# Optimization experiments

Measured on AMD Instinct MI355X. Metric: run time of the kernel, lower is better.

Reference implementation:

```python
import jax, jax.numpy as jnp
import numpy as np

D, L, C, H, W = 4, 16, 64, 128, 128


def setup_inputs() -> dict:
    key = jax.random.key(0)
    ks = jax.random.split(key, 20)
    rn = lambda k, shape, s=0.02: jax.random.normal(k, shape, dtype=jnp.float32) * s
    return {
        "x": jax.random.normal(ks[0], (L, C, H, W), dtype=jnp.float32),
        "ln1_g": jnp.ones((D, C, H, W), jnp.float32),
        "ln1_b": jnp.zeros((D, C, H, W), jnp.float32),
        "Wq": rn(ks[1], (D, C, C)), "bq": jnp.zeros((D, C), jnp.float32),
        "Wk": rn(ks[2], (D, C, C)), "bk": jnp.zeros((D, C), jnp.float32),
        "Wv": rn(ks[3], (D, C, C)), "bv": jnp.zeros((D, C), jnp.float32),
        "Wa": rn(ks[4], (D, 1, 2 * C, 5, 5)), "ba": jnp.zeros((D, 1), jnp.float32),
        "ln2_g": jnp.ones((D, C, H, W), jnp.float32),
        "ln2_b": jnp.zeros((D, C, H, W), jnp.float32),
        "W1": rn(ks[5], (D, 2 * C, C)), "b1": jnp.zeros((D, 2 * C), jnp.float32),
        "W2": rn(ks[6], (D, C, 2 * C)), "b2": jnp.zeros((D, C), jnp.float32),
    }


def _layernorm(x, g, b):
    # torch nn.LayerNorm([C,H,W]): normalize over last 3 dims per frame, eps=1e-5
    mu = jnp.mean(x, axis=(1, 2, 3), keepdims=True)
    var = jnp.var(x, axis=(1, 2, 3), keepdims=True)
    return (x - mu) * jax.lax.rsqrt(var + 1e-5) * g[None] + b[None]


def _conv5(x, w):
    # x: [L, Cin, H, W], w: [1, Cin, 5, 5] -> [L, 1, H, W], SAME padding (pad=2)
    return jax.lax.conv_general_dilated(
        x, w, window_strides=(1, 1), padding="SAME",
        dimension_numbers=("NCHW", "OIHW", "NCHW"))


def _conv1x1(x, w, b):
    # 1x1 conv == per-pixel linear over channels
    return jnp.einsum("lchw,oc->lohw", x, w) + b[None, :, None, None]


def reference(x, ln1_g, ln1_b, Wq, bq, Wk, bk, Wv, bv, Wa, ba,
              ln2_g, ln2_b, W1, b1, W2, b2):
    depth = ln1_g.shape[0]
    c = Wa.shape[2] // 2
    for d in range(depth):
        # --- pre-norm conv attention (nheads=1) + residual ---
        h = _layernorm(x, ln1_g[d], ln1_b[d])
        Q = _conv1x1(h, Wq[d], bq[d])
        K = _conv1x1(h, Wk[d], bk[d])
        V = _conv1x1(h, Wv[d], bv[d])
        # conv_atten(cat([Q_i, K_j])) is linear in channels: split the 5x5
        # kernel into Q-part and K-part, so H_ij = A_i + B_j + bias.
        A = _conv5(Q, Wa[d, :, :c])[:, 0]   # [L, H, W]
        B = _conv5(K, Wa[d, :, c:])[:, 0]   # [L, H, W]
        S = A[:, None] + B[None, :] + ba[d][0]      # [L, L, H, W]
        P = jax.nn.softmax(S, axis=1)               # softmax over source frames j
        attn = jnp.einsum("ijhw,jchw->ichw", P, V)  # weighted sum of V_j
        x = x + attn
        # --- pre-norm conv FFN + residual ---
        h = _layernorm(x, ln2_g[d], ln2_b[d])
        f = _conv1x1(h, W1[d], b1[d])
        f = jax.nn.leaky_relu(f, 0.01)  # torch LeakyReLU default slope
        f = _conv1x1(f, W2[d], b2[d])
        x = x + f
    return x
```

## Files before the change

### kernel.cpp

```cpp
#include <hip/hip_runtime.h>


#define HW 16384
#define CHW 1048576
#define NB 64

typedef unsigned short u16;
typedef __attribute__((ext_vector_type(8))) short bf16x8;
typedef __attribute__((ext_vector_type(8))) unsigned short u16x8;
typedef __attribute__((ext_vector_type(4))) float f32x4;

static __device__ __forceinline__ u16 f2bf(float f) {
  union { float f; unsigned int u; } v; v.f = f;
  unsigned int r = v.u + 0x7fffu + ((v.u >> 16) & 1u);
  return (u16)(r >> 16);
}
static __device__ __forceinline__ float bf2f(u16 h) {
  union { unsigned int u; float f; } v; v.u = ((unsigned int)h) << 16;
  return v.f;
}
static __device__ __forceinline__ void ln_from_acc_wave(
    const float* acc, int l, int lane, float& mu, float& r) {
  const float invN = 1.f / 1048576.f;
  float2 v = *(const float2*)(acc + lane * 32 + 2 * l);
  float s = v.x, q = v.y;
#pragma unroll
  for (int off = 32; off > 0; off >>= 1) {
    s += __shfl_xor(s, off);
    q += __shfl_xor(q, off);
  }
  mu = s * invN;
  r = rsqrtf(q * invN - mu * mu + 1e-5f);
}

__global__ __launch_bounds__(256) void prep_kernel(
    const float* __restrict__ Wa, const float* __restrict__ Wk,
    const float* __restrict__ Wv, const float* __restrict__ W1,
    const float* __restrict__ W2, u16* __restrict__ w1pk,
    u16* __restrict__ w2pk, u16* __restrict__ wvpk, u16* __restrict__ wepk) {
  int d = blockIdx.x;
  int t = blockIdx.y * 256 + threadIdx.x;
  const int STR = 256 * 16;
  const float* WaK = Wa + ((size_t)d * 128 + 64) * 25;
  const float* Wkd = Wk + d * 4096;
  for (int idx = t; idx < 2048; idx += STR) {
    int frag = idx >> 9, lane = (idx >> 3) & 63, j = idx & 7;
    int mt = frag >> 1, kt = frag & 1;
    int tap = mt * 16 + (lane & 15);
    int ci = kt * 32 + (lane >> 4) * 8 + j;
    float s = 0.f;
    if (tap < 25)
      for (int co = 0; co < 64; ++co)
        s = fmaf(WaK[co * 25 + tap], Wkd[co * 64 + ci], s);
    wepk[d * 2048 + idx] = f2bf(s);
  }
  const float* Wvd = Wv + d * 4096;
  for (int idx = t; idx < 4096; idx += STR) {
    int frag = idx >> 9, lane = (idx >> 3) & 63, j = idx & 7;
    int mt = frag >> 1, kt = frag & 1;
    int co = mt * 16 + (lane & 15);
    int ci = kt * 32 + (lane >> 4) * 8 + j;
    wvpk[d * 4096 + idx] = f2bf(Wvd[co * 64 + ci]);
  }
  const float* W1d = W1 + d * 8192;
  for (int idx = t; idx < 8192; idx += STR) {
    int frag = idx >> 9, lane = (idx >> 3) & 63, j = idx & 7;
    int mt = frag >> 1, kt = frag & 1;
    int o = mt * 16 + (lane & 15);
    int ci = kt * 32 + (lane >> 4) * 8 + j;
    w1pk[d * 8192 + idx] = f2bf(W1d[o * 64 + ci]);
  }
  const float* W2d = W2 + d * 8192;
  for (int idx = t; idx < 8192; idx += STR) {
    int frag = idx >> 9, lane = (idx >> 3) & 63, j = idx & 7;
    int mt2 = frag >> 2, kt2 = frag & 3;
    int c = mt2 * 16 + (lane & 15);
    int o = kt2 * 32 + (lane >> 4) * 8 + j;
    w2pk[d * 8192 + idx] = f2bf(W2d[c * 128 + o]);
  }
}

__global__ __launch_bounds__(256) void lngb_kernel(
    const float* __restrict__ g1, u16* __restrict__ o1) {
  int idx = blockIdx.x * 256 + threadIdx.x;
  float4 v = *(const float4*)(g1 + (size_t)idx * 4);
  ushort4 o;
  o.x = f2bf(v.x); o.y = f2bf(v.y); o.z = f2bf(v.z); o.w = f2bf(v.w);
  *(ushort4*)(o1 + (size_t)idx * 4) = o;
}

__global__ __launch_bounds__(256) void stats_kernel(
    const float* __restrict__ xin, float* __restrict__ acc) {
  int tid = threadIdx.x;
  size_t base = (size_t)blockIdx.x * 4096;
  const float4* in4 = (const float4*)(xin + base);
  float s = 0.f, q = 0.f;
#pragma unroll
  for (int k = 0; k < 4; ++k) {
    float4 v = in4[k * 256 + tid];
    s += v.x + v.y + v.z + v.w;
    q = fmaf(v.x, v.x, q); q = fmaf(v.y, v.y, q);
    q = fmaf(v.z, v.z, q); q = fmaf(v.w, v.w, q);
  }
#pragma unroll
  for (int off = 32; off > 0; off >>= 1) {
    s += __shfl_down(s, off); q += __shfl_down(q, off);
  }
  __shared__ float ls[4], lq[4];
  int wave = tid >> 6;
  if ((tid & 63) == 0) { ls[wave] = s; lq[wave] = q; }
  __syncthreads();
  if (tid == 0) {
    int frame = blockIdx.x >> 8;
    int bkt = blockIdx.x & (NB - 1);
    atomicAdd(&acc[bkt * 32 + frame * 2], ls[0] + ls[1] + ls[2] + ls[3]);
    atomicAdd(&acc[bkt * 32 + frame * 2 + 1], lq[0] + lq[1] + lq[2] + lq[3]);
  }
}

__global__ __launch_bounds__(256) void tb_kernel(
    const float* __restrict__ x, const u16* __restrict__ g,
    const float* __restrict__ bln, const u16* __restrict__ wep_g,
    const float* __restrict__ accA, float* __restrict__ accBz,
    float* __restrict__ mulr, u16* __restrict__ T) {
  __shared__ __align__(16) char lds[18432];
  u16* hb = (u16*)lds;
  int tid = threadIdx.x;
  int l = blockIdx.y;
  int p0 = blockIdx.x << 7;
  if (blockIdx.x == 0 && blockIdx.y == 0)
    for (int i = tid; i < NB * 32; i += 256) accBz[i] = 0.f;
  int lane = tid & 63;
  float mu, r;
  ln_from_acc_wave(accA, l, lane, mu, r);
  if (blockIdx.x == 0 && tid == 0) {
    mulr[2 * l] = mu;
    mulr[2 * l + 1] = r;
  }

  {
    int pq = tid & 15, cg = tid >> 4;
    int px0 = pq * 8, c0 = cg * 4;
    float vv[4][8];
#pragma unroll
    for (int i = 0; i < 4; ++i) {
      int c = c0 + i;
      size_t gi = (((size_t)l * 64 + c) << 14) + p0 + px0;
      int li = (c << 14) + p0 + px0;
      float4 xv0 = *(const float4*)(x + gi);
      float4 xv1 = *(const float4*)(x + gi + 4);
      u16x8 gv = *(const u16x8*)(g + li);
      float4 bb0 = *(const float4*)(bln + li);
      float4 bb1 = *(const float4*)(bln + li + 4);
#pragma unroll
      for (int k = 0; k < 8; ++k) {
        float xk = k < 4 ? ((const float*)&xv0)[k] : ((const float*)&xv1)[k - 4];
        float bbk = k < 4 ? ((const float*)&bb0)[k] : ((const float*)&bb1)[k - 4];
        vv[i][k] = (xk - mu) * r * bf2f(gv[k]) + bbk;
      }
    }
#pragma unroll
    for (int k = 0; k < 8; ++k) {
      int row = px0 + k;
      int col = ((((c0 >> 3) + (row >> 2)) & 7) << 3) | (c0 & 7);
      ushort4 hv;
      hv.x = f2bf(vv[0][k]); hv.y = f2bf(vv[1][k]);
      hv.z = f2bf(vv[2][k]); hv.w = f2bf(vv[3][k]);
      *(ushort4*)(hb + row * 72 + col) = hv;
    }
  }
  __syncthreads();

  int wv = tid >> 6;
  int ln15 = lane & 15, quad = lane >> 4;

  bf16x8 ah[2][2];
#pragma unroll
  for (int mt = 0; mt < 2; ++mt) {
    int px = (wv * 2 + mt) * 16 + ln15;
#pragma unroll
    for (int kt = 0; kt < 2; ++kt) {
      int slot = ((kt * 4 + quad) + (px >> 2)) & 7;
      ah[mt][kt] = *(const bf16x8*)(hb + px * 72 + (slot << 3));
    }
  }
  const bf16x8* weg = (const bf16x8*)wep_g;

  f32x4 accT[2][2];
#pragma unroll
  for (int mt = 0; mt < 2; ++mt)
#pragma unroll
    for (int nt = 0; nt < 2; ++nt) accT[mt][nt] = (f32x4){0.f, 0.f, 0.f, 0.f};
#pragma unroll
  for (int nt = 0; nt < 2; ++nt) {
    bf16x8 b0 = weg[(nt * 2 + 0) * 64 + lane];
    bf16x8 b1w = weg[(nt * 2 + 1) * 64 + lane];
#pragma unroll
    for (int mt = 0; mt < 2; ++mt) {
      accT[mt][nt] = __builtin_amdgcn_mfma_f32_16x16x32_bf16(
          ah[mt][0], b0, accT[mt][nt], 0, 0, 0);
      accT[mt][nt] = __builtin_amdgcn_mfma_f32_16x16x32_bf16(
          ah[mt][1], b1w, accT[mt][nt], 0, 0, 0);
    }
  }

#pragma unroll
  for (int mt = 0; mt < 2; ++mt) {
    int pxb = p0 + (wv * 2 + mt) * 16 + quad * 4;
#pragma unroll
    for (int nt = 0; nt < 2; ++nt) {
      int tap = nt * 16 + ln15;
      if (tap < 25) {
        ushort4 o;
        o.x = f2bf(accT[mt][nt][0]); o.y = f2bf(accT[mt][nt][1]);
        o.z = f2bf(accT[mt][nt][2]); o.w = f2bf(accT[mt][nt][3]);
        *(ushort4*)(T + (((size_t)l * 25 + tap) << 14) + pxb) = o;
      }
    }
  }
}

__global__ __launch_bounds__(256) void attnc_kernel(
    const float* __restrict__ x, const u16* __restrict__ T,
    const u16* __restrict__ g1, const float* __restrict__ b1g,
    const u16* __restrict__ wvp_g, const float* __restrict__ bv,
    const float* __restrict__ mulr, u16* __restrict__ abf) {
  __shared__ float Bsm[16][68];
  __shared__ float Prl[16][64];
  __shared__ float scal[64];
  __shared__ __align__(16) u16 hb[64 * 72];
  int tid = threadIdx.x;
  int p0 = blockIdx.x << 6;

  {
    int j = tid >> 4, xg = tid & 15;
    int y0 = p0 >> 7, x0 = p0 & 127;
    float acc4[4] = {0.f, 0.f, 0.f, 0.f};
    const u16* Tj = T + (((size_t)j * 25) << 14);
#pragma unroll
    for (int dy = 0; dy < 5; ++dy) {
      int yy = y0 + dy - 2;
      if (yy < 0 || yy > 127) continue;
#pragma unroll
      for (int dx = 0; dx < 5; ++dx) {
        const u16* Tt = Tj + ((dy * 5 + dx) << 14) + (yy << 7);
#pragma unroll
        for (int k = 0; k < 4; ++k) {
          int xc = x0 + xg * 4 + k + dx - 2;
          if (xc >= 0 && xc < 128) acc4[k] += bf2f(Tt[xc]);
        }
      }
    }
#pragma unroll
    for (int k = 0; k < 4; ++k) Bsm[j][xg * 4 + k] = acc4[k];
  }
  __syncthreads();

  if (tid < 64) {
    float bj[16], m = -1e30f;
#pragma unroll
    for (int j = 0; j < 16; ++j) {
      bj[j] = Bsm[j][tid];
      m = fmaxf(m, bj[j]);
    }
    float sum = 0.f;
#pragma unroll
    for (int j = 0; j < 16; ++j) {
      bj[j] = __expf(bj[j] - m);
      sum += bj[j];
    }
    float inv = 1.f / sum;
    float sc = 0.f;
#pragma unroll
    for (int j = 0; j < 16; ++j) {
      float mu_j = mulr[2 * j], r_j = mulr[2 * j + 1];
      float prl = bj[j] * inv * r_j;
      Prl[j][tid] = prl;
      sc = fmaf(prl, mu_j, sc);
    }
    scal[tid] = sc;
  }
  __syncthreads();

  {
    int c2 = tid >> 3, pxg = tid & 7;
    int px0 = pxg * 8;
    float xbar[2][8];
#pragma unroll
    for (int cc = 0; cc < 2; ++cc)
#pragma unroll
      for (int k = 0; k < 8; ++k) xbar[cc][k] = 0.f;
#pragma unroll
    for (int j = 0; j < 16; ++j) {
      float p8[8];
#pragma unroll
      for (int k = 0; k < 8; ++k) p8[k] = Prl[j][px0 + k];
#pragma unroll
      for (int cc = 0; cc < 2; ++cc) {
        int c = cc * 32 + c2;
        const float* xp = x + (((size_t)j * 64 + c) << 14) + p0 + px0;
        float4 xv0 = *(const float4*)xp;
        float4 xv1 = *(const float4*)(xp + 4);
#pragma unroll
        for (int k = 0; k < 8; ++k) {
          float xk =
              k < 4 ? ((const float*)&xv0)[k] : ((const float*)&xv1)[k - 4];
          xbar[cc][k] = fmaf(p8[k], xk, xbar[cc][k]);
        }
      }
    }
    float sc8[8];
#pragma unroll
    for (int k = 0; k < 8; ++k) sc8[k] = scal[px0 + k];
#pragma unroll
    for (int cc = 0; cc < 2; ++cc) {
      int c = cc * 32 + c2;
      int li = (c << 14) + p0 + px0;
      u16x8 g8 = *(const u16x8*)(g1 + li);
      float4 b0 = *(const float4*)(b1g + li);
      float4 b1v = *(const float4*)(b1g + li + 4);
#pragma unroll
      for (int k = 0; k < 8; ++k) {
        float bbk = k < 4 ? ((const float*)&b0)[k] : ((const float*)&b1v)[k - 4];
        float hv = bf2f(g8[k]) * (xbar[cc][k] - sc8[k]) + bbk;
        int row = px0 + k;
        int col = ((((c >> 3) + (row >> 2)) & 7) << 3) | (c & 7);
        hb[row * 72 + col] = f2bf(hv);
      }
    }
  }
  __syncthreads();

  int wv = tid >> 6, lane = tid & 63;
  int ln15 = lane & 15, quad = lane >> 4;
  int px = wv * 16 + ln15;
  bf16x8 ah[2];
#pragma unroll
  for (int kt = 0; kt < 2; ++kt) {
    int slot = ((kt * 4 + quad) + (px >> 2)) & 7;
    ah[kt] = *(const bf16x8*)(hb + px * 72 + (slot << 3));
  }
  const bf16x8* wvg = (const bf16x8*)wvp_g;
  f32x4 accV[4];
#pragma unroll
  for (int nt = 0; nt < 4; ++nt) accV[nt] = (f32x4){0.f, 0.f, 0.f, 0.f};
#pragma unroll
  for (int nt = 0; nt < 4; ++nt) {
    bf16x8 b0 = wvg[(nt * 2 + 0) * 64 + lane];
    bf16x8 b1w = wvg[(nt * 2 + 1) * 64 + lane];
    accV[nt] = __builtin_amdgcn_mfma_f32_16x16x32_bf16(ah[0], b0, accV[nt],
                                                       0, 0, 0);
    accV[nt] = __builtin_amdgcn_mfma_f32_16x16x32_bf16(ah[1], b1w, accV[nt],
                                                       0, 0, 0);
  }
  int pxb = p0 + wv * 16 + quad * 4;
#pragma unroll
  for (int nt = 0; nt < 4; ++nt) {
    int c = nt * 16 + ln15;
    float bvc = bv[c];
    ushort4 o;
    o.x = f2bf(accV[nt][0] + bvc);
    o.y = f2bf(accV[nt][1] + bvc);
    o.z = f2bf(accV[nt][2] + bvc);
    o.w = f2bf(accV[nt][3] + bvc);
    *(ushort4*)(abf + ((size_t)c << 14) + pxb) = o;
  }
}

__global__ __launch_bounds__(256) void stats2_kernel(
    const float* __restrict__ x, const u16* __restrict__ abf,
    float* __restrict__ accB, float* __restrict__ accAz) {
  int tid = threadIdx.x;
  if (blockIdx.x == 0)
    for (int i = tid; i < NB * 32; i += 256) accAz[i] = 0.f;
  size_t base = (size_t)blockIdx.x * 4096;
  int intra = (blockIdx.x & 255) * 4096;
  float s = 0.f, q = 0.f;
#pragma unroll
  for (int k = 0; k < 4; ++k) {
    int off = (k * 256 + tid) * 4;
    float4 v = *(const float4*)(x + base + off);
    ushort4 a4 = *(const ushort4*)(abf + intra + off);
    float v0 = v.x + bf2f(a4.x), v1 = v.y + bf2f(a4.y);
    float v2 = v.z + bf2f(a4.z), v3 = v.w + bf2f(a4.w);
    s += v0 + v1 + v2 + v3;
    q = fmaf(v0, v0, q); q = fmaf(v1, v1, q);
    q = fmaf(v2, v2, q); q = fmaf(v3, v3, q);
  }
#pragma unroll
  for (int off = 32; off > 0; off >>= 1) {
    s += __shfl_down(s, off); q += __shfl_down(q, off);
  }
  __shared__ float ls[4], lq[4];
  int wave = tid >> 6;
  if ((tid & 63) == 0) { ls[wave] = s; lq[wave] = q; }
  __syncthreads();
  if (tid == 0) {
    int frame = blockIdx.x >> 8;
    int bkt = blockIdx.x & (NB - 1);
    atomicAdd(&accB[bkt * 32 + frame * 2], ls[0] + ls[1] + ls[2] + ls[3]);
    atomicAdd(&accB[bkt * 32 + frame * 2 + 1], lq[0] + lq[1] + lq[2] + lq[3]);
  }
}

__global__ __launch_bounds__(256) void ffn_kernel(
    const float* __restrict__ xr, float* __restrict__ xw,
    const u16* __restrict__ ap, const float* __restrict__ g,
    const float* __restrict__ bln, const u16* __restrict__ w1p_g,
    const float* __restrict__ b1, const u16* __restrict__ w2p_g,
    const float* __restrict__ b2, const float* __restrict__ accB,
    float* __restrict__ accA) {
  __shared__ __align__(16) char lds[66560];
  float* xaf = (float*)lds;
  u16* hb = (u16*)(lds + 33792);
  u16* f1 = (u16*)(lds + 33792);

  int tid = threadIdx.x;
  int P0 = blockIdx.x << 7;
  int l = P0 >> 14;
  int p0 = P0 & 16383;
  int lane = tid & 63;
  float mu, r;
  ln_from_acc_wave(accB, l, lane, mu, r);

#pragma unroll
  for (int it = 0; it < 2; ++it) {
    int pq = tid & 31, cg = (tid >> 5) + it * 8;
    int px = pq * 4, c0 = cg * 4;
    float vv[4][4];
#pragma unroll
    for (int i = 0; i < 4; ++i) {
      int c = c0 + i;
      size_t gi = (((size_t)l * 64 + c) << 14) + p0 + px;
      int li = (c << 14) + p0 + px;
      float4 xv = *(const float4*)(xr + gi);
      ushort4 av4 = *(const ushort4*)(ap + li);
      float4 gv = *(const float4*)(g + li);
      float4 bb = *(const float4*)(bln + li);
      float4 s4;
      s4.x = xv.x + bf2f(av4.x); s4.y = xv.y + bf2f(av4.y);
      s4.z = xv.z + bf2f(av4.z); s4.w = xv.w + bf2f(av4.w);
      *(float4*)(xaf + c * 132 + px) = s4;
      vv[i][0] = (s4.x - mu) * r * gv.x + bb.x;
      vv[i][1] = (s4.y - mu) * r * gv.y + bb.y;
      vv[i][2] = (s4.z - mu) * r * gv.z + bb.z;
      vv[i][3] = (s4.w - mu) * r * gv.w + bb.w;
    }
#pragma unroll
    for (int k = 0; k < 4; ++k) {
      int row = px + k;
      int col = ((((c0 >> 3) + (row >> 2)) & 7) << 3) | (c0 & 7);
      ushort4 hv;
      hv.x = f2bf(vv[0][k]); hv.y = f2bf(vv[1][k]);
      hv.z = f2bf(vv[2][k]); hv.w = f2bf(vv[3][k]);
      *(ushort4*)(hb + row * 72 + col) = hv;
    }
  }
  __syncthreads();

  int wv = tid >> 6;
  int ln15 = lane & 15, quad = lane >> 4;

  bf16x8 bh[2][2];
#pragma unroll
  for (int nt = 0; nt < 2; ++nt) {
    int px = (wv * 2 + nt) * 16 + ln15;
#pragma unroll
    for (int kt = 0; kt < 2; ++kt) {
      int slot = ((kt * 4 + quad) + (px >> 2)) & 7;
      bh[nt][kt] = *(const bf16x8*)(hb + px * 72 + (slot << 3));
    }
  }
  __syncthreads();

  const bf16x8* w1g = (const bf16x8*)w1p_g;
  const bf16x8* w2g = (const bf16x8*)w2p_g;

#pragma unroll
  for (int mt = 0; mt < 8; ++mt) {
    bf16x8 a1a = w1g[(mt * 2 + 0) * 64 + lane];
    bf16x8 a1b = w1g[(mt * 2 + 1) * 64 + lane];
    f32x4 acc[2];
    acc[0] = (f32x4){0.f, 0.f, 0.f, 0.f};
    acc[1] = (f32x4){0.f, 0.f, 0.f, 0.f};
#pragma unroll
    for (int nt = 0; nt < 2; ++nt) {
      acc[nt] = __builtin_amdgcn_mfma_f32_16x16x32_bf16(a1a, bh[nt][0],
                                                        acc[nt], 0, 0, 0);
      acc[nt] = __builtin_amdgcn_mfma_f32_16x16x32_bf16(a1b, bh[nt][1],
                                                        acc[nt], 0, 0, 0);
    }
    int o0 = mt * 16 + quad * 4;
    float4 b1v = *(const float4*)(b1 + o0);
#pragma unroll
    for (int nt = 0; nt < 2; ++nt) {
      int px = (wv * 2 + nt) * 16 + ln15;
      int swz = (px & 7) * 8;
      float fv[4];
#pragma unroll
      for (int rj = 0; rj < 4; ++rj) {
        float f = acc[nt][rj] + ((const float*)&b1v)[rj];
        fv[rj] = fmaxf(f, 0.01f * f);
      }
      int col = ((o0 & ~7) ^ swz) + (o0 & 7);
      ushort4 ov;
      ov.x = f2bf(fv[0]); ov.y = f2bf(fv[1]);
      ov.z = f2bf(fv[2]); ov.w = f2bf(fv[3]);
      *(ushort4*)(f1 + px * 128 + col) = ov;
    }
  }
  __syncthreads();

  bf16x8 a2[2][4];
#pragma unroll
  for (int mt = 0; mt < 2; ++mt) {
    int px = (wv * 2 + mt) * 16 + ln15;
    int swz = (px & 7) * 8;
#pragma unroll
    for (int kt = 0; kt < 4; ++kt)
      a2[mt][kt] =
          *(const bf16x8*)(f1 + px * 128 + ((kt * 32 + quad * 8) ^ swz));
  }
  f32x4 acc2[2][4];
#pragma unroll
  for (int mt = 0; mt < 2; ++mt)
#pragma unroll
    for (int nt = 0; nt < 4; ++nt) acc2[mt][nt] = (f32x4){0.f, 0.f, 0.f, 0.f};
#pragma unroll
  for (int nt = 0; nt < 4; ++nt) {
    bf16x8 bw[4];
#pragma unroll
    for (int kt = 0; kt < 4; ++kt) bw[kt] = w2g[(nt * 4 + kt) * 64 + lane];
#pragma unroll
    for (int mt = 0; mt < 2; ++mt)
#pragma unroll
      for (int kt = 0; kt < 4; ++kt)
        acc2[mt][nt] = __builtin_amdgcn_mfma_f32_16x16x32_bf16(
            a2[mt][kt], bw[kt], acc2[mt][nt], 0, 0, 0);
  }

  float s = 0.f, q = 0.f;
#pragma unroll
  for (int mt = 0; mt < 2; ++mt) {
    int pxl = (wv * 2 + mt) * 16 + quad * 4;
#pragma unroll
    for (int nt = 0; nt < 4; ++nt) {
      int c = nt * 16 + ln15;
      float b2c = b2[c];
      const float* xac = xaf + c * 132 + pxl;
      float4 v;
      v.x = xac[0] + acc2[mt][nt][0] + b2c;
      v.y = xac[1] + acc2[mt][nt][1] + b2c;
      v.z = xac[2] + acc2[mt][nt][2] + b2c;
      v.w = xac[3] + acc2[mt][nt][3] + b2c;
      *(float4*)(xw + (((size_t)l * 64 + c) << 14) + p0 + pxl) = v;
      s += v.x + v.y + v.z + v.w;
      q = fmaf(v.x, v.x, q); q = fmaf(v.y, v.y, q);
      q = fmaf(v.z, v.z, q); q = fmaf(v.w, v.w, q);
    }
  }
#pragma unroll
  for (int off = 32; off > 0; off >>= 1) {
    s += __shfl_down(s, off); q += __shfl_down(q, off);
  }
  if (lane == 0) {
    int bkt = blockIdx.x & (NB - 1);
    atomicAdd(&accA[bkt * 32 + l * 2], s);
    atomicAdd(&accA[bkt * 32 + l * 2 + 1], q);
  }
}

extern "C" void kernel_launch(void* const* d_in, const int* in_sizes, int n_in,
                              void* d_out, int out_size, void* d_ws,
                              size_t ws_size, hipStream_t stream) {
  const float* x_in = (const float*)d_in[0];
  const float* ln1_g = (const float*)d_in[1];
  const float* ln1_b = (const float*)d_in[2];
  const float* Wk = (const float*)d_in[5];
  const float* Wv = (const float*)d_in[7];
  const float* bv = (const float*)d_in[8];
  const float* Wa = (const float*)d_in[9];
  const float* ln2_g = (const float*)d_in[11];
  const float* ln2_b = (const float*)d_in[12];
  const float* W1 = (const float*)d_in[13];
  const float* b1 = (const float*)d_in[14];
  const float* W2 = (const float*)d_in[15];
  const float* b2 = (const float*)d_in[16];

  float* xbuf = (float*)d_out;
  char* wsb = (char*)d_ws;
  u16* T = (u16*)wsb;
  u16* abf = (u16*)(wsb + 13107200);
  u16* g1b = (u16*)(wsb + 15204352);
  u16* w1pk = (u16*)(wsb + 23592960);
  u16* w2pk = (u16*)(wsb + 23658496);
  u16* wvpk = (u16*)(wsb + 23724032);
  u16* wepk = (u16*)(wsb + 23756800);
  float* mulr = (float*)(wsb + 23773184);
  float* accA = (float*)(wsb + 23773312);
  float* accB = (float*)(wsb + 23781504);

  hipMemsetAsync(accA, 0, 16384, stream);
  prep_kernel<<<dim3(4, 16), 256, 0, stream>>>(Wa, Wk, Wv, W1, W2, w1pk, w2pk,
                                               wvpk, wepk);
  lngb_kernel<<<4096, 256, 0, stream>>>(ln1_g, g1b);
  stats_kernel<<<4096, 256, 0, stream>>>(x_in, accA);

  const float* xr = x_in;
  for (int d = 0; d < 4; ++d) {
    tb_kernel<<<dim3(128, 16), 256, 0, stream>>>(
        xr, g1b + (size_t)d * CHW, ln1_b + (size_t)d * CHW, wepk + d * 2048,
        accA, accB, mulr, T);
    attnc_kernel<<<256, 256, 0, stream>>>(
        xr, T, g1b + (size_t)d * CHW, ln1_b + (size_t)d * CHW,
        wvpk + d * 4096, bv + d * 64, mulr, abf);
    stats2_kernel<<<4096, 256, 0, stream>>>(xr, abf, accB, accA);
    ffn_kernel<<<2048, 256, 0, stream>>>(
        xr, xbuf, abf, ln2_g + (size_t)d * CHW, ln2_b + (size_t)d * CHW,
        w1pk + d * 8192, b1 + d * 128, w2pk + d * 8192, b2 + d * 64, accB,
        accA);
    xr = xbuf;
  }
}
```

Before: 569.7 us.

## Switch activations and LN params to channels-last layout across all kernels

Transposes x once into a channels-last (pixel-major, channel-contiguous) workspace buffer and converts all four LayerNorm gamma/beta tensors to channels-last bf16 up front. Each per-layer kernel (tb, attnc, stats2, ffn) now reads and writes contiguous channel vectors per pixel, and the MFMA operands are swapped so outputs land channel-contiguous. The aim is vectorized coalesced loads and simpler LDS staging without per-element transposes, and bf16 beta halves its traffic. The cost is an extra transpose kernel, a larger workspace, a strided channel-major write in the last FFN, and bf16 rounding of the LN biases.

```diff
diff --git a/kernel.cpp b/kernel.cpp
--- a/kernel.cpp
+++ b/kernel.cpp
@@ -4,6 +4,8 @@
 #define HW 16384
 #define CHW 1048576
 #define NB 64
+
+#define XI(l, p, c) ((((size_t)(l)) << 20) + (size_t)(p)*64 + (c))
 
 typedef unsigned short u16;
 typedef __attribute__((ext_vector_type(8))) short bf16x8;
@@ -80,47 +82,100 @@
   }
 }
 
-__global__ __launch_bounds__(256) void lngb_kernel(
-    const float* __restrict__ g1, u16* __restrict__ o1) {
-  int idx = blockIdx.x * 256 + threadIdx.x;
-  float4 v = *(const float4*)(g1 + (size_t)idx * 4);
-  ushort4 o;
-  o.x = f2bf(v.x); o.y = f2bf(v.y); o.z = f2bf(v.z); o.w = f2bf(v.w);
-  *(ushort4*)(o1 + (size_t)idx * 4) = o;
-}
-
-__global__ __launch_bounds__(256) void stats_kernel(
-    const float* __restrict__ xin, float* __restrict__ acc) {
+__global__ __launch_bounds__(256) void pcl_kernel(
+    const float* __restrict__ g1, const float* __restrict__ b1,
+    const float* __restrict__ g2, const float* __restrict__ b2,
+    u16* __restrict__ g1cl, u16* __restrict__ b1cl, u16* __restrict__ g2cl,
+    u16* __restrict__ b2cl) {
+  __shared__ float tl[128][65];
   int tid = threadIdx.x;
-  size_t base = (size_t)blockIdx.x * 4096;
-  const float4* in4 = (const float4*)(xin + base);
+  int y = blockIdx.x;
+  int tsel = blockIdx.y >> 2, d = blockIdx.y & 3;
+  const float* src;
+  u16* dst;
+  switch (tsel) {
+    case 0: src = g1; dst = g1cl; break;
+    case 1: src = b1; dst = b1cl; break;
+    case 2: src = g2; dst = g2cl; break;
+    default: src = b2; dst = b2cl; break;
+  }
+  src += (size_t)d * CHW;
+  dst += (size_t)d * CHW;
+  {
+    int c = tid >> 2, xg = tid & 3;
+    const float* sp = src + (size_t)c * HW + y * 128 + xg * 32;
+#pragma unroll
+    for (int k = 0; k < 8; ++k) {
+      float4 v = *(const float4*)(sp + k * 4);
+      int xx = xg * 32 + k * 4;
+      tl[xx + 0][c] = v.x; tl[xx + 1][c] = v.y;
+      tl[xx + 2][c] = v.z; tl[xx + 3][c] = v.w;
+    }
+  }
+  __syncthreads();
+  {
+    int px = tid >> 1, c0 = (tid & 1) << 5;
+    u16* dp = dst + (size_t)(y * 128 + px) * 64 + c0;
+#pragma unroll
+    for (int k = 0; k < 4; ++k) {
+      u16x8 o;
+#pragma unroll
+      for (int e = 0; e < 8; ++e) o[e] = f2bf(tl[px][c0 + k * 8 + e]);
+      *(u16x8*)(dp + k * 8) = o;
+    }
+  }
+}
+
+__global__ __launch_bounds__(256) void xpose_kernel(
+    const float* __restrict__ xin, float* __restrict__ xcl,
+    float* __restrict__ acc) {
+  __shared__ float tl[128][65];
+  __shared__ float ls[4], lq[4];
+  int tid = threadIdx.x;
+  int l = blockIdx.x >> 7, y = blockIdx.x & 127;
   float s = 0.f, q = 0.f;
-#pragma unroll
-  for (int k = 0; k < 4; ++k) {
-    float4 v = in4[k * 256 + tid];
-    s += v.x + v.y + v.z + v.w;
-    q = fmaf(v.x, v.x, q); q = fmaf(v.y, v.y, q);
-    q = fmaf(v.z, v.z, q); q = fmaf(v.w, v.w, q);
+  {
+    int c = tid >> 2, xg = tid & 3;
+    const float* sp = xin + (size_t)l * CHW + (size_t)c * HW + y * 128 + xg * 32;
+#pragma unroll
+    for (int k = 0; k < 8; ++k) {
+      float4 v = *(const float4*)(sp + k * 4);
+      int xx = xg * 32 + k * 4;
+      tl[xx + 0][c] = v.x; tl[xx + 1][c] = v.y;
+      tl[xx + 2][c] = v.z; tl[xx + 3][c] = v.w;
+      s += v.x + v.y + v.z + v.w;
+      q = fmaf(v.x, v.x, q); q = fmaf(v.y, v.y, q);
+      q = fmaf(v.z, v.z, q); q = fmaf(v.w, v.w, q);
+    }
+  }
+  __syncthreads();
+  {
+    int px = tid >> 1, c0 = (tid & 1) << 5;
+    float* dp = xcl + XI(l, y * 128 + px, c0);
+#pragma unroll
+    for (int k = 0; k < 8; ++k) {
+      float4 w = {tl[px][c0 + k * 4 + 0], tl[px][c0 + k * 4 + 1],
+                  tl[px][c0 + k * 4 + 2], tl[px][c0 + k * 4 + 3]};
+      *(float4*)(dp + k * 4) = w;
+    }
   }
 #pragma unroll
   for (int off = 32; off > 0; off >>= 1) {
     s += __shfl_down(s, off); q += __shfl_down(q, off);
   }
-  __shared__ float ls[4], lq[4];
   int wave = tid >> 6;
   if ((tid & 63) == 0) { ls[wave] = s; lq[wave] = q; }
   __syncthreads();
   if (tid == 0) {
-    int frame = blockIdx.x >> 8;
     int bkt = blockIdx.x & (NB - 1);
-    atomicAdd(&acc[bkt * 32 + frame * 2], ls[0] + ls[1] + ls[2] + ls[3]);
-    atomicAdd(&acc[bkt * 32 + frame * 2 + 1], lq[0] + lq[1] + lq[2] + lq[3]);
+    atomicAdd(&acc[bkt * 32 + l * 2], ls[0] + ls[1] + ls[2] + ls[3]);
+    atomicAdd(&acc[bkt * 32 + l * 2 + 1], lq[0] + lq[1] + lq[2] + lq[3]);
   }
 }
 
 __global__ __launch_bounds__(256) void tb_kernel(
-    const float* __restrict__ x, const u16* __restrict__ g,
-    const float* __restrict__ bln, const u16* __restrict__ wep_g,
+    const float* __restrict__ xcl, const u16* __restrict__ g,
+    const u16* __restrict__ bln, const u16* __restrict__ wep_g,
     const float* __restrict__ accA, float* __restrict__ accBz,
     float* __restrict__ mulr, u16* __restrict__ T) {
   __shared__ __align__(16) char lds[18432];
@@ -139,34 +194,24 @@
   }
 
   {
-    int pq = tid & 15, cg = tid >> 4;
-    int px0 = pq * 8, c0 = cg * 4;
-    float vv[4][8];
-#pragma unroll
-    for (int i = 0; i < 4; ++i) {
-      int c = c0 + i;
-      size_t gi = (((size_t)l * 64 + c) << 14) + p0 + px0;
-      int li = (c << 14) + p0 + px0;
-      float4 xv0 = *(const float4*)(x + gi);
-      float4 xv1 = *(const float4*)(x + gi + 4);
-      u16x8 gv = *(const u16x8*)(g + li);
-      float4 bb0 = *(const float4*)(bln + li);
-      float4 bb1 = *(const float4*)(bln + li + 4);
-#pragma unroll
-      for (int k = 0; k < 8; ++k) {
-        float xk = k < 4 ? ((const float*)&xv0)[k] : ((const float*)&xv1)[k - 4];
-        float bbk = k < 4 ? ((const float*)&bb0)[k] : ((const float*)&bb1)[k - 4];
-        vv[i][k] = (xk - mu) * r * bf2f(gv[k]) + bbk;
+    int px = tid >> 1, cs = (tid & 1) << 5;
+    const float* xp = xcl + XI(l, p0 + px, cs);
+    size_t pb = (size_t)(p0 + px) * 64 + cs;
+#pragma unroll
+    for (int ch = 0; ch < 4; ++ch) {
+      float4 xv0 = *(const float4*)(xp + ch * 8);
+      float4 xv1 = *(const float4*)(xp + ch * 8 + 4);
+      u16x8 g8 = *(const u16x8*)(g + pb + ch * 8);
+      u16x8 b8 = *(const u16x8*)(bln + pb + ch * 8);
+      u16x8 hv;
+#pragma unroll
+      for (int e = 0; e < 8; ++e) {
+        float xk = e < 4 ? ((const float*)&xv0)[e] : ((const float*)&xv1)[e - 4];
+        hv[e] = f2bf((xk - mu) * r * bf2f(g8[e]) + bf2f(b8[e]));
       }
-    }
-#pragma unroll
-    for (int k = 0; k < 8; ++k) {
-      int row = px0 + k;
-      int col = ((((c0 >> 3) + (row >> 2)) & 7) << 3) | (c0 & 7);
-      ushort4 hv;
-      hv.x = f2bf(vv[0][k]); hv.y = f2bf(vv[1][k]);
-      hv.z = f2bf(vv[2][k]); hv.w = f2bf(vv[3][k]);
-      *(ushort4*)(hb + row * 72 + col) = hv;
+      int ch_abs = (cs >> 3) + ch;
+      int slot = (ch_abs + (px >> 2)) & 7;
+      *(u16x8*)(hb + px * 72 + slot * 8) = hv;
     }
   }
   __syncthreads();
@@ -221,8 +266,8 @@
 }
 
 __global__ __launch_bounds__(256) void attnc_kernel(
-    const float* __restrict__ x, const u16* __restrict__ T,
-    const u16* __restrict__ g1, const float* __restrict__ b1g,
+    const float* __restrict__ xcl, const u16* __restrict__ T,
+    const u16* __restrict__ g1, const u16* __restrict__ b1g,
     const u16* __restrict__ wvp_g, const float* __restrict__ bv,
     const float* __restrict__ mulr, u16* __restrict__ abf) {
   __shared__ float Bsm[16][68];
@@ -283,50 +328,40 @@
   __syncthreads();
 
   {
-    int c2 = tid >> 3, pxg = tid & 7;
-    int px0 = pxg * 8;
-    float xbar[2][8];
-#pragma unroll
-    for (int cc = 0; cc < 2; ++cc)
-#pragma unroll
-      for (int k = 0; k < 8; ++k) xbar[cc][k] = 0.f;
+    int pxl = tid >> 2, qq = tid & 3;
+    int c0 = qq << 4;
+    float xb16[16];
+#pragma unroll
+    for (int e = 0; e < 16; ++e) xb16[e] = 0.f;
 #pragma unroll
     for (int j = 0; j < 16; ++j) {
-      float p8[8];
-#pragma unroll
-      for (int k = 0; k < 8; ++k) p8[k] = Prl[j][px0 + k];
-#pragma unroll
-      for (int cc = 0; cc < 2; ++cc) {
-        int c = cc * 32 + c2;
-        const float* xp = x + (((size_t)j * 64 + c) << 14) + p0 + px0;
-        float4 xv0 = *(const float4*)xp;
-        float4 xv1 = *(const float4*)(xp + 4);
-#pragma unroll
-        for (int k = 0; k < 8; ++k) {
-          float xk =
-              k < 4 ? ((const float*)&xv0)[k] : ((const float*)&xv1)[k - 4];
-          xbar[cc][k] = fmaf(p8[k], xk, xbar[cc][k]);
-        }
+      float p = Prl[j][pxl];
+      const float* xp = xcl + XI(j, p0 + pxl, c0);
+      float4 v0 = *(const float4*)xp;
+      float4 v1 = *(const float4*)(xp + 4);
+      float4 v2 = *(const float4*)(xp + 8);
+      float4 v3 = *(const float4*)(xp + 12);
+#pragma unroll
+      for (int e = 0; e < 4; ++e) {
+        xb16[e] = fmaf(p, ((const float*)&v0)[e], xb16[e]);
+        xb16[4 + e] = fmaf(p, ((const float*)&v1)[e], xb16[4 + e]);
+        xb16[8 + e] = fmaf(p, ((const float*)&v2)[e], xb16[8 + e]);
+        xb16[12 + e] = fmaf(p, ((const float*)&v3)[e], xb16[12 + e]);
       }
     }
-    float sc8[8];
-#pragma unroll
-    for (int k = 0; k < 8; ++k) sc8[k] = scal[px0 + k];
-#pragma unroll
-    for (int cc = 0; cc < 2; ++cc) {
-      int c = cc * 32 + c2;
-      int li = (c << 14) + p0 + px0;
-      u16x8 g8 = *(const u16x8*)(g1 + li);
-      float4 b0 = *(const float4*)(b1g + li);
-      float4 b1v = *(const float4*)(b1g + li + 4);
-#pragma unroll
-      for (int k = 0; k < 8; ++k) {
-        float bbk = k < 4 ? ((const float*)&b0)[k] : ((const float*)&b1v)[k - 4];
-        float hv = bf2f(g8[k]) * (xbar[cc][k] - sc8[k]) + bbk;
-        int row = px0 + k;
-        int col = ((((c >> 3) + (row >> 2)) & 7) << 3) | (c & 7);
-        hb[row * 72 + col] = f2bf(hv);
-      }
+    float sc = scal[pxl];
+    size_t pb = (size_t)(p0 + pxl) * 64 + c0;
+#pragma unroll
+    for (int ch = 0; ch < 2; ++ch) {
+      u16x8 g8 = *(const u16x8*)(g1 + pb + ch * 8);
+      u16x8 b8 = *(const u16x8*)(b1g + pb + ch * 8);
+      u16x8 hv;
+#pragma unroll
+      for (int e = 0; e < 8; ++e)
+        hv[e] = f2bf(bf2f(g8[e]) * (xb16[ch * 8 + e] - sc) + bf2f(b8[e]));
+      int ch_abs = (c0 >> 3) + ch;
+      int slot = (ch_abs + (pxl >> 2)) & 7;
+      *(u16x8*)(hb + pxl * 72 + slot * 8) = hv;
     }
   }
   __syncthreads();
@@ -346,41 +381,41 @@
   for (int nt = 0; nt < 4; ++nt) accV[nt] = (f32x4){0.f, 0.f, 0.f, 0.f};
 #pragma unroll
   for (int nt = 0; nt < 4; ++nt) {
-    bf16x8 b0 = wvg[(nt * 2 + 0) * 64 + lane];
-    bf16x8 b1w = wvg[(nt * 2 + 1) * 64 + lane];
-    accV[nt] = __builtin_amdgcn_mfma_f32_16x16x32_bf16(ah[0], b0, accV[nt],
+    bf16x8 w0 = wvg[(nt * 2 + 0) * 64 + lane];
+    bf16x8 w1w = wvg[(nt * 2 + 1) * 64 + lane];
+    accV[nt] = __builtin_amdgcn_mfma_f32_16x16x32_bf16(w0, ah[0], accV[nt],
                                                        0, 0, 0);
-    accV[nt] = __builtin_amdgcn_mfma_f32_16x16x32_bf16(ah[1], b1w, accV[nt],
+    accV[nt] = __builtin_amdgcn_mfma_f32_16x16x32_bf16(w1w, ah[1], accV[nt],
                                                        0, 0, 0);
   }
-  int pxb = p0 + wv * 16 + quad * 4;
+  size_t pbase = (size_t)(p0 + wv * 16 + ln15) * 64;
 #pragma unroll
   for (int nt = 0; nt < 4; ++nt) {
-    int c = nt * 16 + ln15;
-    float bvc = bv[c];
+    int c0 = nt * 16 + quad * 4;
+    float4 bvv = *(const float4*)(bv + c0);
     ushort4 o;
-    o.x = f2bf(accV[nt][0] + bvc);
-    o.y = f2bf(accV[nt][1] + bvc);
-    o.z = f2bf(accV[nt][2] + bvc);
-    o.w = f2bf(accV[nt][3] + bvc);
-    *(ushort4*)(abf + ((size_t)c << 14) + pxb) = o;
+    o.x = f2bf(accV[nt][0] + bvv.x);
+    o.y = f2bf(accV[nt][1] + bvv.y);
+    o.z = f2bf(accV[nt][2] + bvv.z);
+    o.w = f2bf(accV[nt][3] + bvv.w);
+    *(ushort4*)(abf + pbase + c0) = o;
   }
 }
 
 __global__ __launch_bounds__(256) void stats2_kernel(
-    const float* __restrict__ x, const u16* __restrict__ abf,
+    const float* __restrict__ xcl, const u16* __restrict__ abf,
     float* __restrict__ accB, float* __restrict__ accAz) {
   int tid = threadIdx.x;
   if (blockIdx.x == 0)
     for (int i = tid; i < NB * 32; i += 256) accAz[i] = 0.f;
-  size_t base = (size_t)blockIdx.x * 4096;
-  int intra = (blockIdx.x & 255) * 4096;
+  int l = blockIdx.x >> 8;
+  int o0 = (blockIdx.x & 255) * 4096;
   float s = 0.f, q = 0.f;
 #pragma unroll
   for (int k = 0; k < 4; ++k) {
-    int off = (k * 256 + tid) * 4;
-    float4 v = *(const float4*)(x + base + off);
-    ushort4 a4 = *(const ushort4*)(abf + intra + off);
+    int o = o0 + (k * 256 + tid) * 4;
+    float4 v = *(const float4*)(xcl + (((size_t)l) << 20) + o);
+    ushort4 a4 = *(const ushort4*)(abf + o);
     float v0 = v.x + bf2f(a4.x), v1 = v.y + bf2f(a4.y);
     float v2 = v.z + bf2f(a4.z), v3 = v.w + bf2f(a4.w);
     s += v0 + v1 + v2 + v3;
@@ -396,64 +431,61 @@
   if ((tid & 63) == 0) { ls[wave] = s; lq[wave] = q; }
   __syncthreads();
   if (tid == 0) {
-    int frame = blockIdx.x >> 8;
     int bkt = blockIdx.x & (NB - 1);
-    atomicAdd(&accB[bkt * 32 + frame * 2], ls[0] + ls[1] + ls[2] + ls[3]);
-    atomicAdd(&accB[bkt * 32 + frame * 2 + 1], lq[0] + lq[1] + lq[2] + lq[3]);
+    atomicAdd(&accB[bkt * 32 + l * 2], ls[0] + ls[1] + ls[2] + ls[3]);
+    atomicAdd(&accB[bkt * 32 + l * 2 + 1], lq[0] + lq[1] + lq[2] + lq[3]);
   }
 }
 
 __global__ __launch_bounds__(256) void ffn_kernel(
-    const float* __restrict__ xr, float* __restrict__ xw,
-    const u16* __restrict__ ap, const float* __restrict__ g,
-    const float* __restrict__ bln, const u16* __restrict__ w1p_g,
+    float* __restrict__ xcl, float* __restrict__ xout_cm,
+    const u16* __restrict__ ap, const u16* __restrict__ g,
+    const u16* __restrict__ bln, const u16* __restrict__ w1p_g,
     const float* __restrict__ b1, const u16* __restrict__ w2p_g,
     const float* __restrict__ b2, const float* __restrict__ accB,
-    float* __restrict__ accA) {
-  __shared__ __align__(16) char lds[66560];
+    float* __restrict__ accA, int cmaj, int dostats) {
+  __shared__ __align__(16) char lds[67584];
   float* xaf = (float*)lds;
-  u16* hb = (u16*)(lds + 33792);
-  u16* f1 = (u16*)(lds + 33792);
+  u16* hb = (u16*)(lds + 34816);
+  u16* f1 = (u16*)(lds + 34816);
 
   int tid = threadIdx.x;
-  int P0 = blockIdx.x << 7;
-  int l = P0 >> 14;
-  int p0 = P0 & 16383;
+  int l = blockIdx.x >> 7;
+  int y0 = blockIdx.x & 127;
+  int p0 = y0 << 7;
   int lane = tid & 63;
   float mu, r;
   ln_from_acc_wave(accB, l, lane, mu, r);
 
-#pragma unroll
-  for (int it = 0; it < 2; ++it) {
-    int pq = tid & 31, cg = (tid >> 5) + it * 8;
-    int px = pq * 4, c0 = cg * 4;
-    float vv[4][4];
-#pragma unroll
-    for (int i = 0; i < 4; ++i) {
-      int c = c0 + i;
-      size_t gi = (((size_t)l * 64 + c) << 14) + p0 + px;
-      int li = (c << 14) + p0 + px;
-      float4 xv = *(const float4*)(xr + gi);
-      ushort4 av4 = *(const ushort4*)(ap + li);
-      float4 gv = *(const float4*)(g + li);
-      float4 bb = *(const float4*)(bln + li);
-      float4 s4;
-      s4.x = xv.x + bf2f(av4.x); s4.y = xv.y + bf2f(av4.y);
-      s4.z = xv.z + bf2f(av4.z); s4.w = xv.w + bf2f(av4.w);
-      *(float4*)(xaf + c * 132 + px) = s4;
-      vv[i][0] = (s4.x - mu) * r * gv.x + bb.x;
-      vv[i][1] = (s4.y - mu) * r * gv.y + bb.y;
-      vv[i][2] = (s4.z - mu) * r * gv.z + bb.z;
-      vv[i][3] = (s4.w - mu) * r * gv.w + bb.w;
-    }
-#pragma unroll
-    for (int k = 0; k < 4; ++k) {
-      int row = px + k;
-      int col = ((((c0 >> 3) + (row >> 2)) & 7) << 3) | (c0 & 7);
-      ushort4 hv;
-      hv.x = f2bf(vv[0][k]); hv.y = f2bf(vv[1][k]);
-      hv.z = f2bf(vv[2][k]); hv.w = f2bf(vv[3][k]);
-      *(ushort4*)(hb + row * 72 + col) = hv;
+  {
+    int px = tid >> 1, cs = (tid & 1) << 5;
+    const float* xp = xcl + XI(l, p0 + px, cs);
+    size_t pb = (size_t)(p0 + px) * 64 + cs;
+    float* xr = xaf + px * 68 + cs;
+#pragma unroll
+    for (int ch = 0; ch < 4; ++ch) {
+      float4 xv0 = *(const float4*)(xp + ch * 8);
+      float4 xv1 = *(const float4*)(xp + ch * 8 + 4);
+      u16x8 a8 = *(const u16x8*)(ap + pb + ch * 8);
+      u16x8 g8 = *(const u16x8*)(g + pb + ch * 8);
+      u16x8 b8 = *(const u16x8*)(bln + pb + ch * 8);
+      float xa[8];
+#pragma unroll
+      for (int e = 0; e < 8; ++e) {
+        float xk = e < 4 ? ((const float*)&xv0)[e] : ((const float*)&xv1)[e - 4];
+        xa[e] = xk + bf2f(a8[e]);
+      }
+      float4 w0 = {xa[0], xa[1], xa[2], xa[3]};
+      float4 w1 = {xa[4], xa[5], xa[6], xa[7]};
+      *(float4*)(xr + ch * 8) = w0;
+      *(float4*)(xr + ch * 8 + 4) = w1;
+      u16x8 hv;
+#pragma unroll
+      for (int e = 0; e < 8; ++e)
+        hv[e] = f2bf((xa[e] - mu) * r * bf2f(g8[e]) + bf2f(b8[e]));
+      int ch_abs = (cs >> 3) + ch;
+      int slot = (ch_abs + (px >> 2)) & 7;
+      *(u16x8*)(hb + px * 72 + slot * 8) = hv;
     }
   }
   __syncthreads();
@@ -536,37 +568,48 @@
 #pragma unroll
       for (int kt = 0; kt < 4; ++kt)
         acc2[mt][nt] = __builtin_amdgcn_mfma_f32_16x16x32_bf16(
-            a2[mt][kt], bw[kt], acc2[mt][nt], 0, 0, 0);
+            bw[kt], a2[mt][kt], acc2[mt][nt], 0, 0, 0);
   }
 
   float s = 0.f, q = 0.f;
 #pragma unroll
   for (int mt = 0; mt < 2; ++mt) {
-    int pxl = (wv * 2 + mt) * 16 + quad * 4;
+    int pxl = (wv * 2 + mt) * 16 + ln15;
 #pragma unroll
     for (int nt = 0; nt < 4; ++nt) {
-      int c = nt * 16 + ln15;
-      float b2c = b2[c];
-      const float* xac = xaf + c * 132 + pxl;
+      int c0 = nt * 16 + quad * 4;
+      float4 b2v = *(const float4*)(b2 + c0);
+      const float* xac = xaf + pxl * 68 + c0;
+      float4 xav = *(const float4*)xac;
       float4 v;
-      v.x = xac[0] + acc2[mt][nt][0] + b2c;
-      v.y = xac[1] + acc2[mt][nt][1] + b2c;
-      v.z = xac[2] + acc2[mt][nt][2] + b2c;
-      v.w = xac[3] + acc2[mt][nt][3] + b2c;
-      *(float4*)(xw + (((size_t)l * 64 + c) << 14) + p0 + pxl) = v;
+      v.x = xav.x + acc2[mt][nt][0] + b2v.x;
+      v.y = xav.y + acc2[mt][nt][1] + b2v.y;
+      v.z = xav.z + acc2[mt][nt][2] + b2v.z;
+      v.w = xav.w + acc2[mt][nt][3] + b2v.w;
+      if (cmaj) {
+        size_t ob = (size_t)l * CHW + p0 + pxl + (size_t)c0 * HW;
+        xout_cm[ob] = v.x;
+        xout_cm[ob + HW] = v.y;
+        xout_cm[ob + 2 * HW] = v.z;
+        xout_cm[ob + 3 * HW] = v.w;
+      } else {
+        *(float4*)(xcl + XI(l, p0 + pxl, c0)) = v;
+      }
       s += v.x + v.y + v.z + v.w;
       q = fmaf(v.x, v.x, q); q = fmaf(v.y, v.y, q);
       q = fmaf(v.z, v.z, q); q = fmaf(v.w, v.w, q);
     }
   }
-#pragma unroll
-  for (int off = 32; off > 0; off >>= 1) {
-    s += __shfl_down(s, off); q += __shfl_down(q, off);
-  }
-  if (lane == 0) {
-    int bkt = blockIdx.x & (NB - 1);
-    atomicAdd(&accA[bkt * 32 + l * 2], s);
-    atomicAdd(&accA[bkt * 32 + l * 2 + 1], q);
+  if (dostats) {
+#pragma unroll
+    for (int off = 32; off > 0; off >>= 1) {
+      s += __shfl_down(s, off); q += __shfl_down(q, off);
+    }
+    if (lane == 0) {
+      int bkt = blockIdx.x & (NB - 1);
+      atomicAdd(&accA[bkt * 32 + l * 2], s);
+      atomicAdd(&accA[bkt * 32 + l * 2 + 1], q);
+    }
   }
 }
 
@@ -589,36 +632,39 @@
 
   float* xbuf = (float*)d_out;
   char* wsb = (char*)d_ws;
-  u16* T = (u16*)wsb;
-  u16* abf = (u16*)(wsb + 13107200);
-  u16* g1b = (u16*)(wsb + 15204352);
-  u16* w1pk = (u16*)(wsb + 23592960);
-  u16* w2pk = (u16*)(wsb + 23658496);
-  u16* wvpk = (u16*)(wsb + 23724032);
-  u16* wepk = (u16*)(wsb + 23756800);
-  float* mulr = (float*)(wsb + 23773184);
-  float* accA = (float*)(wsb + 23773312);
-  float* accB = (float*)(wsb + 23781504);
+  float* xcl = (float*)wsb;
+  u16* T = (u16*)(wsb + 67108864);
+  u16* abf = (u16*)(wsb + 80216064);
+  u16* g1cl = (u16*)(wsb + 82313216);
+  u16* b1cl = (u16*)(wsb + 90701824);
+  u16* g2cl = (u16*)(wsb + 99090432);
+  u16* b2cl = (u16*)(wsb + 107479040);
+  u16* w1pk = (u16*)(wsb + 115867648);
+  u16* w2pk = (u16*)(wsb + 115933184);
+  u16* wvpk = (u16*)(wsb + 115998720);
+  u16* wepk = (u16*)(wsb + 116031488);
+  float* mulr = (float*)(wsb + 116047872);
+  float* accA = (float*)(wsb + 116048000);
+  float* accB = (float*)(wsb + 116056192);
 
   hipMemsetAsync(accA, 0, 16384, stream);
   prep_kernel<<<dim3(4, 16), 256, 0, stream>>>(Wa, Wk, Wv, W1, W2, w1pk, w2pk,
                                                wvpk, wepk);
-  lngb_kernel<<<4096, 256, 0, stream>>>(ln1_g, g1b);
-  stats_kernel<<<4096, 256, 0, stream>>>(x_in, accA);
-
-  const float* xr = x_in;
+  pcl_kernel<<<dim3(128, 16), 256, 0, stream>>>(ln1_g, ln1_b, ln2_g, ln2_b,
+                                                g1cl, b1cl, g2cl, b2cl);
+  xpose_kernel<<<2048, 256, 0, stream>>>(x_in, xcl, accA);
+
   for (int d = 0; d < 4; ++d) {
     tb_kernel<<<dim3(128, 16), 256, 0, stream>>>(
-        xr, g1b + (size_t)d * CHW, ln1_b + (size_t)d * CHW, wepk + d * 2048,
+        xcl, g1cl + (size_t)d * CHW, b1cl + (size_t)d * CHW, wepk + d * 2048,
         accA, accB, mulr, T);
     attnc_kernel<<<256, 256, 0, stream>>>(
-        xr, T, g1b + (size_t)d * CHW, ln1_b + (size_t)d * CHW,
+        xcl, T, g1cl + (size_t)d * CHW, b1cl + (size_t)d * CHW,
         wvpk + d * 4096, bv + d * 64, mulr, abf);
-    stats2_kernel<<<4096, 256, 0, stream>>>(xr, abf, accB, accA);
+    stats2_kernel<<<4096, 256, 0, stream>>>(xcl, abf, accB, accA);
     ffn_kernel<<<2048, 256, 0, stream>>>(
-        xr, xbuf, abf, ln2_g + (size_t)d * CHW, ln2_b + (size_t)d * CHW,
+        xcl, xbuf, abf, g2cl + (size_t)d * CHW, b2cl + (size_t)d * CHW,
         w1pk + d * 8192, b1 + d * 128, w2pk + d * 8192, b2 + d * 64, accB,
-        accA);
-    xr = xbuf;
-  }
-}
+        accA, d == 3 ? 1 : 0, d < 3 ? 1 : 0);
+  }
+}
```

After: 648.2 us. +13.8%, slower.
